# Performance work log

Hardware: AMD Instinct MI355X
Metric: run time of the kernel (lower is better)

Reference implementation:

```python
import jax, jax.numpy as jnp
import numpy as np

Z_RANGE = 1.0

def calc_rho(f):
    # camera distance along z so that the unit object fills the image plane
    return 2.0 * f

def rt_to_homo(rot, t):
    # rot: (N,3,3), t: (N,3,1) -> (N,4,4) [R t; 0 0 0 1]
    N = rot.shape[0]
    top = jnp.concatenate([rot, t], axis=-1)
    bottom = jnp.broadcast_to(jnp.array([0.0, 0.0, 0.0, 1.0], rot.dtype), (N, 1, 4))
    return jnp.concatenate([top, bottom], axis=1)

def diag_to_homo(s):
    # s: (N,3) -> (N,4,4) diag(s1,s2,s3,1)
    N = s.shape[0]
    d = jnp.concatenate([s, jnp.ones((N, 1), s.dtype)], axis=-1)
    return jax.vmap(jnp.diag)(d)

def grid_sample_3d(vox, grid):
    # vox: (N,C,D,H,W); grid: (N,Do,Ho,Wo,3) with (x,y,z) in [-1,1]
    # trilinear, align_corners=True, zero padding (torch F.grid_sample defaults)
    N, C, D, H, W = vox.shape
    Do, Ho, Wo = grid.shape[1], grid.shape[2], grid.shape[3]
    P = Do * Ho * Wo
    x = (grid[..., 0] + 1.0) * 0.5 * (W - 1)
    y = (grid[..., 1] + 1.0) * 0.5 * (H - 1)
    z = (grid[..., 2] + 1.0) * 0.5 * (D - 1)
    x0 = jnp.floor(x); y0 = jnp.floor(y); z0 = jnp.floor(z)
    vox_flat = vox.reshape(N, C, D * H * W)
    out = jnp.zeros((N, C, P), vox.dtype)
    for dz in (0, 1):
        for dy in (0, 1):
            for dx in (0, 1):
                ix = x0 + dx; iy = y0 + dy; iz = z0 + dz
                w = (1.0 - jnp.abs(x - ix)) * (1.0 - jnp.abs(y - iy)) * (1.0 - jnp.abs(z - iz))
                valid = (ix >= 0) & (ix <= W - 1) & (iy >= 0) & (iy <= H - 1) & (iz >= 0) & (iz <= D - 1)
                w = jnp.where(valid, w, 0.0)
                ixc = jnp.clip(ix, 0, W - 1).astype(jnp.int32)
                iyc = jnp.clip(iy, 0, H - 1).astype(jnp.int32)
                izc = jnp.clip(iz, 0, D - 1).astype(jnp.int32)
                idx = ((izc * H + iyc) * W + ixc).reshape(N, 1, P)
                vals = jnp.take_along_axis(vox_flat, idx, axis=2)  # (N,C,P)
                out = out + vals * w.reshape(N, 1, P)
    return out.reshape(N, C, Do, Ho, Wo)

def get_world2camera(scale, trans, rot, f):
    trans = trans.at[..., -1].set(calc_rho(f))          # overwrite z with rho
    rot_T = jnp.swapaxes(rot, 1, 2)                      # R^T
    rt = rt_to_homo(rot_T, trans[..., None])             # (N,4,4)
    cTw = jnp.matmul(rt, diag_to_homo(scale))            # (N,4,4)
    return cTw

def world_grid(out_size, out_depth, dtype=jnp.float32):
    xs = jnp.linspace(-0.5, 0.5, out_size, dtype=dtype)
    zs = jnp.linspace(-0.5, 0.5, out_depth, dtype=dtype)
    zg, yg, xg = jnp.meshgrid(zs, xs, xs, indexing='ij')  # (Do,S,S)
    return jnp.stack([xg, yg, zg, jnp.ones_like(xg)], axis=-1)  # (Do,S,S,4)

def camera2ray_grid(cgrid, f):
    # cgrid: (N,Do,H,W,4) homogeneous camera coords
    N = cgrid.shape[0]
    g = cgrid[..., 0:3] / cgrid[..., 3:4]
    fz = f.reshape(N, 1, 1, 1)
    rho = calc_rho(f).reshape(N, 1, 1, 1)
    x = fz * g[..., 0] / g[..., 2]
    y = fz * g[..., 1] / g[..., 2]
    z = g[..., 2] - rho
    return jnp.stack([2.0 * x, 2.0 * y, 2.0 * z / Z_RANGE], axis=-1)

def setup_inputs() -> dict:
    key = jax.random.key(0)
    k0, k1, k2, k3, k4 = jax.random.split(key, 5)
    N, C, Din = 4, 16, 64
    voxels = jax.random.normal(k0, (N, C, Din, Din, Din), jnp.float32)
    scale = 0.8 + 0.4 * jax.random.uniform(k1, (N, 3), jnp.float32)
    trans = 0.1 * jax.random.normal(k2, (N, 3), jnp.float32)
    A = jax.random.normal(k3, (N, 3, 3), jnp.float32)
    rot, _ = jnp.linalg.qr(A)  # proper orthonormal frames
    f = 1.0 + jax.random.uniform(k4, (N,), jnp.float32)
    return {"voxels": voxels, "scale": scale, "trans": trans, "rot": rot,
            "f": f, "out_size": 128, "out_depth": 64}

def reference(voxels, scale, trans, rot, f, out_size, out_depth):
    # backproj path (forward default: inv=False)
    N = voxels.shape[0]
    cTw = get_world2camera(scale, trans, rot, f)                   # (N,4,4)
    wgrid = world_grid(out_size, out_depth, voxels.dtype)          # (Do,S,S,4)
    cgrid = jnp.einsum('dhwk,njk->ndhwj', wgrid, cTw)              # (N,Do,S,S,4)
    rgrid = camera2ray_grid(cgrid, f)                              # (N,Do,S,S,3)
    return grid_sample_3d(voxels, rgrid)
```

## Files before the change

### kernel.cpp

```cpp
#include <hip/hip_runtime.h>
#include <hip/hip_fp16.h>

#define SS   128
#define DOUT 64
#define DIN  64
#define NC   16
#define NB   4
#define VOXN (DIN*DIN*DIN)

typedef __attribute__((ext_vector_type(4))) unsigned int uint4v;

__global__ __launch_bounds__(256) void transpose_h_kernel(
    const float* __restrict__ vox, __half* __restrict__ wst)
{
    const int tid = blockIdx.x * 256 + threadIdx.x;
    const float* src = vox + ((size_t)(tid >> 18)) * (NC * VOXN) + (tid & (VOXN - 1));

    unsigned int u[8];
    #pragma unroll
    for (int c = 0; c < 8; ++c) {
        const float a = src[(size_t)(2*c)   * VOXN];
        const float b = src[(size_t)(2*c+1) * VOXN];
        const __half2 h = __floats2half2_rn(a, b);
        u[c] = *(const unsigned int*)&h;
    }
    uint4v* dst = (uint4v*)(wst + (size_t)tid * NC);
    dst[0] = (uint4v){u[0], u[1], u[2], u[3]};
    dst[1] = (uint4v){u[4], u[5], u[6], u[7]};
}

__global__ __launch_bounds__(256) void persp3d_h8_kernel(
    const __half* __restrict__ wst,
    const float* __restrict__ scale,
    const float* __restrict__ trans,
    const float* __restrict__ rot,
    const float* __restrict__ fp,
    float* __restrict__ out)
{
    const int bid  = blockIdx.x;
    const int lbid = ((bid & 7) << 12) | (bid >> 3);
    const int t   = threadIdx.x;
    const int chh = t & 1;
    const int w   = t >> 1;
    const int h   = lbid & (SS - 1);
    const int d   = (lbid >> 7) & (DOUT - 1);
    const int n   = lbid >> 13;

    const float fv  = fp[n];
    const float rho = 2.0f * fv;
    const float s0 = scale[n*3+0], s1 = scale[n*3+1], s2 = scale[n*3+2];
    const float tx = trans[n*3+0], ty = trans[n*3+1];
    const float* R = rot + n*9;

    const float px = -0.5f + (float)w * (1.0f/(SS - 1));
    const float py = -0.5f + (float)h * (1.0f/(SS - 1));
    const float pz = -0.5f + (float)d * (1.0f/(DOUT - 1));

    const float cx = R[0]*s0*px + R[3]*s1*py + R[6]*s2*pz + tx;
    const float cy = R[1]*s0*px + R[4]*s1*py + R[7]*s2*pz + ty;
    const float cz = R[2]*s0*px + R[5]*s1*py + R[8]*s2*pz + rho;

    const float inv = 1.0f / cz;
    const float gx = 2.0f * fv * cx * inv;
    const float gy = 2.0f * fv * cy * inv;
    const float gz = 2.0f * (cz - rho);

    const float vx = (gx + 1.0f) * (0.5f * (DIN - 1));
    const float vy = (gy + 1.0f) * (0.5f * (DIN - 1));
    const float vz = (gz + 1.0f) * (0.5f * (DIN - 1));

    const float x0f = floorf(vx), y0f = floorf(vy), z0f = floorf(vz);
    const int   x0  = (int)x0f,   y0  = (int)y0f,   z0  = (int)z0f;
    const float fx = vx - x0f, fy = vy - y0f, fz = vz - z0f;

    float wx[2], wy[2], wz[2];
    int   xi[2], yi[2], zi[2];
    #pragma unroll
    for (int k = 0; k < 2; ++k) {
        const int ix = x0 + k, iy = y0 + k, iz = z0 + k;
        wx[k] = (ix >= 0 && ix < DIN) ? (k ? fx : 1.0f - fx) : 0.0f;
        wy[k] = (iy >= 0 && iy < DIN) ? (k ? fy : 1.0f - fy) : 0.0f;
        wz[k] = (iz >= 0 && iz < DIN) ? (k ? fz : 1.0f - fz) : 0.0f;
        xi[k] = min(max(ix, 0), DIN - 1);
        yi[k] = min(max(iy, 0), DIN - 1);
        zi[k] = min(max(iz, 0), DIN - 1);
    }

    const __half* vb = wst + (size_t)n * VOXN * NC + chh * 8;

    float acc[8];
    #pragma unroll
    for (int c = 0; c < 8; ++c) acc[c] = 0.0f;

    #pragma unroll
    for (int kz = 0; kz < 2; ++kz)
      #pragma unroll
      for (int ky = 0; ky < 2; ++ky)
        #pragma unroll
        for (int kx = 0; kx < 2; ++kx) {
            const float wgt = wz[kz] * wy[ky] * wx[kx];
            const int   idx = (zi[kz]*DIN + yi[ky])*DIN + xi[kx];
            const uint4v r = *(const uint4v*)(vb + (size_t)idx * NC);
            #pragma unroll
            for (int j = 0; j < 4; ++j) {
                const unsigned int uu = r[j];
                const float2 f2 = __half22float2(*(const __half2*)&uu);
                acc[2*j+0] += wgt * f2.x;
                acc[2*j+1] += wgt * f2.y;
            }
        }

    float* ob = out + (((size_t)(n*NC + chh*8)*DOUT + d)*SS + h)*SS + w;
    #pragma unroll
    for (int j = 0; j < 8; ++j)
        __builtin_nontemporal_store(acc[j], ob + (size_t)j * (DOUT*SS*SS));
}

__global__ __launch_bounds__(256) void persp3d_kernel(
    const float* __restrict__ vox,
    const float* __restrict__ scale,
    const float* __restrict__ trans,
    const float* __restrict__ rot,
    const float* __restrict__ fp,
    float* __restrict__ out)
{
    const int tid = blockIdx.x * 256 + threadIdx.x;
    const int w = tid & (SS - 1);
    const int h = (tid >> 7) & (SS - 1);
    const int d = (tid >> 14) & (DOUT - 1);
    const int n = tid >> 20;

    const float fv  = fp[n];
    const float rho = 2.0f * fv;
    const float s0 = scale[n*3+0], s1 = scale[n*3+1], s2 = scale[n*3+2];
    const float tx = trans[n*3+0], ty = trans[n*3+1];
    const float* R = rot + n*9;

    const float px = -0.5f + (float)w * (1.0f/(SS - 1));
    const float py = -0.5f + (float)h * (1.0f/(SS - 1));
    const float pz = -0.5f + (float)d * (1.0f/(DOUT - 1));

    const float cx = R[0]*s0*px + R[3]*s1*py + R[6]*s2*pz + tx;
    const float cy = R[1]*s0*px + R[4]*s1*py + R[7]*s2*pz + ty;
    const float cz = R[2]*s0*px + R[5]*s1*py + R[8]*s2*pz + rho;

    const float inv = 1.0f / cz;
    const float gx = 2.0f * fv * cx * inv;
    const float gy = 2.0f * fv * cy * inv;
    const float gz = 2.0f * (cz - rho);

    const float vx = (gx + 1.0f) * (0.5f * (DIN - 1));
    const float vy = (gy + 1.0f) * (0.5f * (DIN - 1));
    const float vz = (gz + 1.0f) * (0.5f * (DIN - 1));

    const float x0f = floorf(vx), y0f = floorf(vy), z0f = floorf(vz);
    const int   x0  = (int)x0f,   y0  = (int)y0f,   z0  = (int)z0f;
    const float fx = vx - x0f, fy = vy - y0f, fz = vz - z0f;

    float wx[2], wy[2], wz[2];
    int   xi[2], yi[2], zi[2];
    #pragma unroll
    for (int k = 0; k < 2; ++k) {
        const int ix = x0 + k, iy = y0 + k, iz = z0 + k;
        wx[k] = (ix >= 0 && ix < DIN) ? (k ? fx : 1.0f - fx) : 0.0f;
        wy[k] = (iy >= 0 && iy < DIN) ? (k ? fy : 1.0f - fy) : 0.0f;
        wz[k] = (iz >= 0 && iz < DIN) ? (k ? fz : 1.0f - fz) : 0.0f;
        xi[k] = min(max(ix, 0), DIN - 1);
        yi[k] = min(max(iy, 0), DIN - 1);
        zi[k] = min(max(iz, 0), DIN - 1);
    }

    int   idx[8];
    float wgt[8];
    #pragma unroll
    for (int kz = 0; kz < 2; ++kz)
      #pragma unroll
      for (int ky = 0; ky < 2; ++ky)
        #pragma unroll
        for (int kx = 0; kx < 2; ++kx) {
            const int k = (kz << 2) | (ky << 1) | kx;
            idx[k] = (zi[kz]*DIN + yi[ky])*DIN + xi[kx];
            wgt[k] = wz[kz]*wy[ky]*wx[kx];
        }

    const float* vb = vox + (size_t)n * NC * VOXN;
    float*       ob = out + (((size_t)(n*NC)*DOUT + d)*SS + h)*SS + w;

    #pragma unroll 4
    for (int c = 0; c < NC; ++c) {
        const float* vc = vb + (size_t)c * VOXN;
        float acc = 0.0f;
        #pragma unroll
        for (int k = 0; k < 8; ++k)
            acc += wgt[k] * vc[idx[k]];
        ob[(size_t)c * (DOUT*SS*SS)] = acc;
    }
}

extern "C" void kernel_launch(void* const* d_in, const int* in_sizes, int n_in,
                              void* d_out, int out_size, void* d_ws, size_t ws_size,
                              hipStream_t stream) {
    const float* vox   = (const float*)d_in[0];
    const float* scale = (const float*)d_in[1];
    const float* trans = (const float*)d_in[2];
    const float* rot   = (const float*)d_in[3];
    const float* f     = (const float*)d_in[4];
    float* out = (float*)d_out;

    const size_t need = (size_t)NB * VOXN * NC * sizeof(__half);

    if (ws_size >= need) {
        __half* wst = (__half*)d_ws;
        const int tblocks = (NB * VOXN) / 256;
        transpose_h_kernel<<<tblocks, 256, 0, stream>>>(vox, wst);
        const int sblocks = NB * DOUT * SS;
        persp3d_h8_kernel<<<sblocks, 256, 0, stream>>>(wst, scale, trans, rot, f, out);
    } else {
        const int blocks = (NB * DOUT * SS * SS) / 256;
        persp3d_kernel<<<blocks, 256, 0, stream>>>(vox, scale, trans, rot, f, out);
    }
}
```

Before: 89.58 us.

## Compute all 16 channels per thread and use nontemporal loads in transpose

The sampling kernel now assigns one output point to each thread and accumulates all 16 channels, instead of splitting channels across two lanes. This halves the thread count and removes the duplicated coordinate and weight math. Each block now covers two rows of 128 points, and the block index is remapped to match. The transpose kernel also reads its input with nontemporal loads to avoid polluting the cache. In exchange, each thread holds more registers (16 accumulators plus two 16-byte loads per corner), which may lower occupancy and reduce latency hiding for the gathers.

```diff
diff --git a/kernel.cpp b/kernel.cpp
--- a/kernel.cpp
+++ b/kernel.cpp
@@ -19,8 +19,8 @@
     unsigned int u[8];
     #pragma unroll
     for (int c = 0; c < 8; ++c) {
-        const float a = src[(size_t)(2*c)   * VOXN];
-        const float b = src[(size_t)(2*c+1) * VOXN];
+        const float a = __builtin_nontemporal_load(src + (size_t)(2*c)   * VOXN);
+        const float b = __builtin_nontemporal_load(src + (size_t)(2*c+1) * VOXN);
         const __half2 h = __floats2half2_rn(a, b);
         u[c] = *(const unsigned int*)&h;
     }
@@ -29,7 +29,7 @@
     dst[1] = (uint4v){u[4], u[5], u[6], u[7]};
 }
 
-__global__ __launch_bounds__(256) void persp3d_h8_kernel(
+__global__ __launch_bounds__(256) void persp3d_c16_kernel(
     const __half* __restrict__ wst,
     const float* __restrict__ scale,
     const float* __restrict__ trans,
@@ -38,13 +38,13 @@
     float* __restrict__ out)
 {
     const int bid  = blockIdx.x;
-    const int lbid = ((bid & 7) << 12) | (bid >> 3);
-    const int t   = threadIdx.x;
-    const int chh = t & 1;
-    const int w   = t >> 1;
-    const int h   = lbid & (SS - 1);
-    const int d   = (lbid >> 7) & (DOUT - 1);
-    const int n   = lbid >> 13;
+    const int lbid = ((bid & 7) << 11) | (bid >> 3);
+    const int t  = threadIdx.x;
+    const int w  = t & (SS - 1);
+    const int hh = t >> 7;
+    const int h  = ((lbid & 63) << 1) | hh;
+    const int d  = (lbid >> 6) & (DOUT - 1);
+    const int n  = lbid >> 12;
 
     const float fv  = fp[n];
     const float rho = 2.0f * fv;
@@ -86,11 +86,11 @@
         zi[k] = min(max(iz, 0), DIN - 1);
     }
 
-    const __half* vb = wst + (size_t)n * VOXN * NC + chh * 8;
-
-    float acc[8];
-    #pragma unroll
-    for (int c = 0; c < 8; ++c) acc[c] = 0.0f;
+    const __half* vb = wst + (size_t)n * VOXN * NC;
+
+    float acc[NC];
+    #pragma unroll
+    for (int c = 0; c < NC; ++c) acc[c] = 0.0f;
 
     #pragma unroll
     for (int kz = 0; kz < 2; ++kz)
@@ -100,20 +100,26 @@
         for (int kx = 0; kx < 2; ++kx) {
             const float wgt = wz[kz] * wy[ky] * wx[kx];
             const int   idx = (zi[kz]*DIN + yi[ky])*DIN + xi[kx];
-            const uint4v r = *(const uint4v*)(vb + (size_t)idx * NC);
+            const __half* cp = vb + (size_t)idx * NC;
+            const uint4v r0 = *(const uint4v*)cp;
+            const uint4v r1 = *(const uint4v*)(cp + 8);
             #pragma unroll
             for (int j = 0; j < 4; ++j) {
-                const unsigned int uu = r[j];
-                const float2 f2 = __half22float2(*(const __half2*)&uu);
-                acc[2*j+0] += wgt * f2.x;
-                acc[2*j+1] += wgt * f2.y;
+                const unsigned int u0 = r0[j];
+                const unsigned int u1 = r1[j];
+                const float2 f0 = __half22float2(*(const __half2*)&u0);
+                const float2 f1 = __half22float2(*(const __half2*)&u1);
+                acc[2*j+0] += wgt * f0.x;
+                acc[2*j+1] += wgt * f0.y;
+                acc[8+2*j+0] += wgt * f1.x;
+                acc[8+2*j+1] += wgt * f1.y;
             }
         }
 
-    float* ob = out + (((size_t)(n*NC + chh*8)*DOUT + d)*SS + h)*SS + w;
-    #pragma unroll
-    for (int j = 0; j < 8; ++j)
-        __builtin_nontemporal_store(acc[j], ob + (size_t)j * (DOUT*SS*SS));
+    float* ob = out + (((size_t)(n*NC)*DOUT + d)*SS + h)*SS + w;
+    #pragma unroll
+    for (int c = 0; c < NC; ++c)
+        __builtin_nontemporal_store(acc[c], ob + (size_t)c * (DOUT*SS*SS));
 }
 
 __global__ __launch_bounds__(256) void persp3d_kernel(
@@ -213,8 +219,8 @@
         __half* wst = (__half*)d_ws;
         const int tblocks = (NB * VOXN) / 256;
         transpose_h_kernel<<<tblocks, 256, 0, stream>>>(vox, wst);
-        const int sblocks = NB * DOUT * SS;
-        persp3d_h8_kernel<<<sblocks, 256, 0, stream>>>(wst, scale, trans, rot, f, out);
+        const int sblocks = (NB * DOUT * SS * SS) / 256;
+        persp3d_c16_kernel<<<sblocks, 256, 0, stream>>>(wst, scale, trans, rot, f, out);
     } else {
         const int blocks = (NB * DOUT * SS * SS) / 256;
         persp3d_kernel<<<blocks, 256, 0, stream>>>(vox, scale, trans, rot, f, out);
```

Measured after the change: 96.68 us. 1.08x slower.
